# Kernel optimization log

Measured on AMD Instinct MI355X. Metric: run time of the kernel, lower is better.

The kernel has to match this reference:

```python
import jax, jax.numpy as jnp
import numpy as np

T, N, G2, R, E, I, O = 20, 512, 16, 128, 64, 2, 5


def setup_inputs() -> dict:
    key = jax.random.key(0)
    ks = jax.random.split(key, 12)
    s = 0.02
    return {
        "nodes": jax.random.normal(ks[0], (T, N, I), jnp.float32),
        "grids": jax.random.uniform(ks[1], (T, N, N, G2), jnp.float32),
        "hidden_states": jnp.zeros((N, R), jnp.float32),
        "cell_states": jnp.zeros((N, R), jnp.float32),
        "W_in": jax.random.normal(ks[2], (E, I), jnp.float32) * s,
        "b_in": jnp.zeros((E,), jnp.float32),
        "W_tensor": jax.random.normal(ks[3], (E, G2 * R), jnp.float32) * s,
        "b_tensor": jnp.zeros((E,), jnp.float32),
        "W_ih": jax.random.normal(ks[4], (4 * R, 2 * E), jnp.float32) * s,
        "b_ih": jnp.zeros((4 * R,), jnp.float32),
        "W_hh": jax.random.normal(ks[5], (4 * R, R), jnp.float32) * s,
        "b_hh": jnp.zeros((4 * R,), jnp.float32),
        "W_out": jax.random.normal(ks[6], (O, R), jnp.float32) * s,
        "b_out": jnp.zeros((O,), jnp.float32),
    }


def reference(nodes, grids, hidden_states, cell_states,
              W_in, b_in, W_tensor, b_tensor,
              W_ih, b_ih, W_hh, b_hh, W_out, b_out):
    def step(carry, xs):
        h, c = carry
        nodes_t, grid_t = xs  # [N,I], [N,N,G2]
        # social tensor: for each node, grid[node].T @ hidden -> [N, G2, R]
        social = jnp.einsum('nmg,mr->ngr', grid_t, h).reshape(N, G2 * R)
        ie = jax.nn.relu(nodes_t @ W_in.T + b_in)          # [N,E]
        te = jax.nn.relu(social @ W_tensor.T + b_tensor)   # [N,E]
        x = jnp.concatenate([ie, te], axis=1)              # [N,2E]
        gates = x @ W_ih.T + b_ih + h @ W_hh.T + b_hh      # [N,4R]
        i_g, f_g, g_g, o_g = jnp.split(gates, 4, axis=1)   # torch LSTMCell order
        c2 = jax.nn.sigmoid(f_g) * c + jax.nn.sigmoid(i_g) * jnp.tanh(g_g)
        h2 = jax.nn.sigmoid(o_g) * jnp.tanh(c2)
        out = h2 @ W_out.T + b_out                         # [N,O]
        return (h2, c2), out

    (h_f, c_f), outputs = jax.lax.scan(step, (hidden_states, cell_states), (nodes, grids))
    return outputs, h_f, c_f
```

## Files before the change

kernel.cpp:

```cpp
#include <hip/hip_runtime.h>

#define TT 20
#define NNODE 512
#define G2C 16
#define RCH 128
#define ECH 64
#define ICH 2
#define OCH 5
#define KSOC 8192
#define KSPLIT 16
#define KCH 512
#define SGS 516

#define OFF_H    0u
#define OFF_C    65536u
#define OFF_HT   131072u
#define OFF_PART 655360u
#define OFF_WCAT 1179648u
#define OFF_WTT  1310720u
#define OFF_BS   1441792u

__device__ __forceinline__ double sigd(double x){ return 1.0/(1.0+exp(-x)); }

__global__ void k_init(const float* __restrict__ h0, const float* __restrict__ c0,
                       const float* __restrict__ W_ih, const float* __restrict__ b_ih,
                       const float* __restrict__ W_hh, const float* __restrict__ b_hh,
                       const float* __restrict__ W_tensor, double* __restrict__ ws) {
  int tid = blockIdx.x*blockDim.x + threadIdx.x;
  int nthr = gridDim.x*blockDim.x;
  double* h = ws + OFF_H; double* c = ws + OFF_C;
  double* Wcat = ws + OFF_WCAT; double* WtT = ws + OFF_WTT;
  double* bs = ws + OFF_BS;
  for (int i = tid; i < NNODE*RCH; i += nthr) { h[i] = (double)h0[i]; c[i] = (double)c0[i]; }
  for (int i = tid; i < 512*256; i += nthr) {
    int kk = i & 255; int gc = i >> 8;
    Wcat[i] = (kk < 128) ? (double)W_ih[gc*128 + kk] : (double)W_hh[gc*128 + (kk-128)];
  }
  for (int i = tid; i < 2048*64; i += nthr) {
    int e = i & 63; int q2 = i >> 6;
    WtT[i] = (double)W_tensor[e*2048 + q2];
  }
  for (int i = tid; i < 512; i += nthr) bs[i] = (double)b_ih[i] + (double)b_hh[i];
}

__global__ __launch_bounds__(256) void k_social(const float* __restrict__ grids,
                                                double* __restrict__ ws, int t) {
  __shared__ __align__(16) double sgd[4160];
  float* sgf = (float*)sgd;
  const double* __restrict__ Ht = ws + OFF_HT;
  double* __restrict__ part = ws + OFF_PART;
  const int kc = blockIdx.x & (KSPLIT-1);
  const int n0 = (blockIdx.x >> 4) << 4;
  const int kb = kc * KCH;
  const int tid = threadIdx.x;
  const float* gbase = grids + (size_t)t*NNODE*KSOC;
  for (int i = tid; i < 16*128; i += 256) {
    int row = i >> 7; int c4 = i & 127;
    float4 v = *(const float4*)(gbase + (size_t)(n0+row)*KSOC + kb + (c4<<2));
    *(float4*)(&sgf[row*SGS + (c4<<2)]) = v;
  }
  __syncthreads();
  const int lane = tid & 63;
  const int wv = tid >> 6;
  const int e0 = (lane & 15) << 2;
  const int nq = lane >> 4;
  double acc[4][4] = {};
  const int kl0 = wv << 7;
  const double* htp = Ht + (size_t)(kb + kl0)*ECH + e0;
  #pragma unroll 2
  for (int kk = 0; kk < 128; kk += 2) {
    double2 b0a = *(const double2*)(htp + (size_t)kk*ECH);
    double2 b0b = *(const double2*)(htp + (size_t)kk*ECH + 2);
    double2 b1a = *(const double2*)(htp + (size_t)(kk+1)*ECH);
    double2 b1b = *(const double2*)(htp + (size_t)(kk+1)*ECH + 2);
    const int kl = kl0 + kk;
    #pragma unroll
    for (int jn = 0; jn < 4; ++jn) {
      float2 av2 = *(const float2*)(&sgf[((jn<<2)+nq)*SGS + kl]);
      double a0 = (double)av2.x, a1 = (double)av2.y;
      acc[jn][0] += a0*b0a.x + a1*b1a.x;
      acc[jn][1] += a0*b0a.y + a1*b1a.y;
      acc[jn][2] += a0*b0b.x + a1*b1b.x;
      acc[jn][3] += a0*b0b.y + a1*b1b.y;
    }
  }
  __syncthreads();
  if (wv > 0) {
    double* rp = sgd + ((size_t)(wv-1)*64 + lane)*16;
    #pragma unroll
    for (int jn = 0; jn < 4; ++jn)
      #pragma unroll
      for (int je = 0; je < 4; ++je) rp[(jn<<2)+je] = acc[jn][je];
  }
  __syncthreads();
  if (wv == 0) {
    #pragma unroll
    for (int w = 0; w < 3; ++w) {
      const double* rp = sgd + ((size_t)w*64 + lane)*16;
      #pragma unroll
      for (int jn = 0; jn < 4; ++jn)
        #pragma unroll
        for (int je = 0; je < 4; ++je) acc[jn][je] += rp[(jn<<2)+je];
    }
    #pragma unroll
    for (int jn = 0; jn < 4; ++jn) {
      double* pp = part + ((size_t)kc*NNODE + n0 + (jn<<2) + nq)*ECH + e0;
      pp[0]=acc[jn][0]; pp[1]=acc[jn][1]; pp[2]=acc[jn][2]; pp[3]=acc[jn][3];
    }
  }
}

__global__ __launch_bounds__(256) void k_cell(const float* __restrict__ nodes,
    const float* __restrict__ W_in, const float* __restrict__ b_in,
    const float* __restrict__ b_tensor,
    double* __restrict__ ws, float* __restrict__ hf, float* __restrict__ cf, int t) {
  __shared__ double xh[16][258];
  __shared__ double gbuf[32][17];
  double* __restrict__ h = ws + OFF_H;
  double* __restrict__ c = ws + OFF_C;
  const double* __restrict__ part = ws + OFF_PART;
  const double* __restrict__ Wcat = ws + OFF_WCAT;
  const double* __restrict__ bs = ws + OFF_BS;
  const int tid = threadIdx.x;
  const int nc = blockIdx.x >> 4;
  const int rc = blockIdx.x & 15;
  const int m0 = nc << 4;
  {
    const int e = tid & 63;
    #pragma unroll
    for (int pass = 0; pass < 4; ++pass) {
      const int n = (tid >> 6) + (pass << 2);
      const int m = m0 + n;
      double te = (double)b_tensor[e];
      for (int kc = 0; kc < KSPLIT; ++kc)
        te += part[((size_t)kc*NNODE + m)*ECH + e];
      double n0v = (double)nodes[((size_t)t*NNODE + m)*ICH + 0];
      double n1v = (double)nodes[((size_t)t*NNODE + m)*ICH + 1];
      double ie = n0v*(double)W_in[e*2] + n1v*(double)W_in[e*2+1] + (double)b_in[e];
      xh[n][e] = fmax(ie, 0.0);
      xh[n][64+e] = fmax(te, 0.0);
    }
    const int r = tid & 127;
    #pragma unroll
    for (int pass = 0; pass < 8; ++pass) {
      const int n = (tid >> 7) + (pass << 1);
      xh[n][128+r] = h[(size_t)(m0+n)*RCH + r];
    }
  }
  __syncthreads();
  {
    const int n = tid & 15, tg = tid >> 4;
    const int q0 = tg >> 3, jr = tg & 7;
    const int gc0 = q0*128 + rc*8 + jr;
    const int gc1 = (q0+2)*128 + rc*8 + jr;
    const double* w0 = Wcat + (size_t)gc0*256;
    const double* w1 = Wcat + (size_t)gc1*256;
    double a0 = 0.0, a1 = 0.0;
    #pragma unroll 8
    for (int kk = 0; kk < 256; kk += 2) {
      double2 xv = *(const double2*)(&xh[n][kk]);
      double2 wa = *(const double2*)(w0 + kk);
      double2 wb = *(const double2*)(w1 + kk);
      a0 += xv.x*wa.x + xv.y*wa.y;
      a1 += xv.x*wb.x + xv.y*wb.y;
    }
    gbuf[tg][n]    = a0 + bs[gc0];
    gbuf[tg+16][n] = a1 + bs[gc1];
  }
  __syncthreads();
  if (tid < 128) {
    const int n = tid >> 3, jr = tid & 7;
    const int m = m0 + n, r = rc*8 + jr;
    double ig = sigd(gbuf[jr][n]);
    double fg = sigd(gbuf[8+jr][n]);
    double gg = tanh(gbuf[16+jr][n]);
    double og = sigd(gbuf[24+jr][n]);
    double cold = c[(size_t)m*RCH + r];
    double c2 = fg*cold + ig*gg;
    double h2v = og*tanh(c2);
    c[(size_t)m*RCH + r] = c2;
    h[(size_t)m*RCH + r] = h2v;
    if (t == TT-1) {
      hf[(size_t)m*RCH + r] = (float)h2v;
      cf[(size_t)m*RCH + r] = (float)c2;
    }
  }
}

__global__ __launch_bounds__(256) void k_ht_out(const float* __restrict__ W_out,
    const float* __restrict__ b_out, double* __restrict__ ws,
    float* __restrict__ outp, int t, int wout) {
  __shared__ double h2b[16][130];
  const double* __restrict__ h = ws + OFF_H;
  const double* __restrict__ WtT = ws + OFF_WTT;
  double* __restrict__ Ht = ws + OFF_HT;
  const int tid = threadIdx.x;
  const int mc = blockIdx.x >> 3;
  const int gc2 = blockIdx.x & 7;
  const int m0 = mc << 4, g0 = gc2 << 1;
  {
    const int r = tid & 127;
    #pragma unroll
    for (int pass = 0; pass < 8; ++pass) {
      const int n = (tid >> 7) + (pass << 1);
      h2b[n][r] = h[(size_t)(m0+n)*RCH + r];
    }
  }
  __syncthreads();
  {
    const int e = tid & 63, mh = tid >> 6;
    const double* wt0 = WtT + (size_t)(g0*128)*ECH + e;
    const double* wt1 = WtT + (size_t)((g0+1)*128)*ECH + e;
    double acc[4][2] = {};
    #pragma unroll 4
    for (int rr = 0; rr < 128; ++rr) {
      double w0 = wt0[(size_t)rr*ECH];
      double w1 = wt1[(size_t)rr*ECH];
      #pragma unroll
      for (int mi = 0; mi < 4; ++mi) {
        double hv = h2b[(mh<<2)+mi][rr];
        acc[mi][0] += hv*w0;
        acc[mi][1] += hv*w1;
      }
    }
    #pragma unroll
    for (int mi = 0; mi < 4; ++mi) {
      const int m = m0 + (mh<<2) + mi;
      Ht[((size_t)m*G2C + g0    )*ECH + e] = acc[mi][0];
      Ht[((size_t)m*G2C + g0 + 1)*ECH + e] = acc[mi][1];
    }
  }
  if (gc2 == 0 && wout && tid < 80) {
    const int mi = tid / OCH, oo = tid % OCH;
    double v = (double)b_out[oo];
    for (int r = 0; r < 128; ++r)
      v += h2b[mi][r]*(double)W_out[oo*RCH + r];
    outp[((size_t)t*NNODE + m0 + mi)*OCH + oo] = (float)v;
  }
}

extern "C" void kernel_launch(void* const* d_in, const int* in_sizes, int n_in,
                              void* d_out, int out_size, void* d_ws, size_t ws_size,
                              hipStream_t stream) {
  const float* nodes    = (const float*)d_in[0];
  const float* grids    = (const float*)d_in[1];
  const float* h0       = (const float*)d_in[2];
  const float* c0       = (const float*)d_in[3];
  const float* W_in     = (const float*)d_in[4];
  const float* b_in     = (const float*)d_in[5];
  const float* W_tensor = (const float*)d_in[6];
  const float* b_tensor = (const float*)d_in[7];
  const float* W_ih     = (const float*)d_in[8];
  const float* b_ih     = (const float*)d_in[9];
  const float* W_hh     = (const float*)d_in[10];
  const float* b_hh     = (const float*)d_in[11];
  const float* W_out    = (const float*)d_in[12];
  const float* b_out    = (const float*)d_in[13];
  double* ws = (double*)d_ws;
  float* outp = (float*)d_out;
  float* hf = outp + (size_t)TT*NNODE*OCH;
  float* cf = hf + (size_t)NNODE*RCH;

  k_init<<<256, 256, 0, stream>>>(h0, c0, W_ih, b_ih, W_hh, b_hh, W_tensor, ws);
  k_ht_out<<<256, 256, 0, stream>>>(W_out, b_out, ws, outp, 0, 0);
  for (int t = 0; t < TT; ++t) {
    k_social<<<512, 256, 0, stream>>>(grids, ws, t);
    k_cell<<<512, 256, 0, stream>>>(nodes, W_in, b_in, b_tensor, ws, hf, cf, t);
    k_ht_out<<<256, 256, 0, stream>>>(W_out, b_out, ws, outp, t, 1);
  }
}
```

Baseline: 1.397 ms.

## Fuse per-step kernels into one persistent kernel with atomic grid barriers

Replaces the 61 per-timestep kernel launches (social, cell, ht_out) with one persistent 512-block kernel that loops over timesteps and separates phases with a global atomic-counter barrier. The Ht projection is also remapped to one g-slice per block across 512 blocks, and it is skipped on the last step. This removes launch overhead and inter-kernel gaps. In exchange, all 512 blocks must be co-resident, since otherwise the spin barrier deadlocks, and the barriers add spin and fence costs.

```diff
diff --git a/kernel.cpp b/kernel.cpp
--- a/kernel.cpp
+++ b/kernel.cpp
@@ -11,6 +11,7 @@
 #define KSPLIT 16
 #define KCH 512
 #define SGS 516
+#define NBLK 512
 
 #define OFF_H    0u
 #define OFF_C    65536u
@@ -19,6 +20,7 @@
 #define OFF_WCAT 1179648u
 #define OFF_WTT  1310720u
 #define OFF_BS   1441792u
+#define OFF_BAR  1442304u
 
 __device__ __forceinline__ double sigd(double x){ return 1.0/(1.0+exp(-x)); }
 
@@ -31,6 +33,7 @@
   double* h = ws + OFF_H; double* c = ws + OFF_C;
   double* Wcat = ws + OFF_WCAT; double* WtT = ws + OFF_WTT;
   double* bs = ws + OFF_BS;
+  if (tid == 0) { unsigned* bar = (unsigned*)(ws + OFF_BAR); bar[0] = 0u; bar[1] = 0u; }
   for (int i = tid; i < NNODE*RCH; i += nthr) { h[i] = (double)h0[i]; c[i] = (double)c0[i]; }
   for (int i = tid; i < 512*256; i += nthr) {
     int kk = i & 255; int gc = i >> 8;
@@ -43,199 +46,237 @@
   for (int i = tid; i < 512; i += nthr) bs[i] = (double)b_ih[i] + (double)b_hh[i];
 }
 
-__global__ __launch_bounds__(256) void k_social(const float* __restrict__ grids,
-                                                double* __restrict__ ws, int t) {
-  __shared__ __align__(16) double sgd[4160];
-  float* sgf = (float*)sgd;
-  const double* __restrict__ Ht = ws + OFF_HT;
-  double* __restrict__ part = ws + OFF_PART;
-  const int kc = blockIdx.x & (KSPLIT-1);
-  const int n0 = (blockIdx.x >> 4) << 4;
-  const int kb = kc * KCH;
-  const int tid = threadIdx.x;
-  const float* gbase = grids + (size_t)t*NNODE*KSOC;
-  for (int i = tid; i < 16*128; i += 256) {
-    int row = i >> 7; int c4 = i & 127;
-    float4 v = *(const float4*)(gbase + (size_t)(n0+row)*KSOC + kb + (c4<<2));
-    *(float4*)(&sgf[row*SGS + (c4<<2)]) = v;
-  }
+__device__ __forceinline__ void grid_sync(unsigned* bar, unsigned gen) {
   __syncthreads();
-  const int lane = tid & 63;
-  const int wv = tid >> 6;
-  const int e0 = (lane & 15) << 2;
-  const int nq = lane >> 4;
-  double acc[4][4] = {};
-  const int kl0 = wv << 7;
-  const double* htp = Ht + (size_t)(kb + kl0)*ECH + e0;
-  #pragma unroll 2
-  for (int kk = 0; kk < 128; kk += 2) {
-    double2 b0a = *(const double2*)(htp + (size_t)kk*ECH);
-    double2 b0b = *(const double2*)(htp + (size_t)kk*ECH + 2);
-    double2 b1a = *(const double2*)(htp + (size_t)(kk+1)*ECH);
-    double2 b1b = *(const double2*)(htp + (size_t)(kk+1)*ECH + 2);
-    const int kl = kl0 + kk;
-    #pragma unroll
-    for (int jn = 0; jn < 4; ++jn) {
-      float2 av2 = *(const float2*)(&sgf[((jn<<2)+nq)*SGS + kl]);
-      double a0 = (double)av2.x, a1 = (double)av2.y;
-      acc[jn][0] += a0*b0a.x + a1*b1a.x;
-      acc[jn][1] += a0*b0a.y + a1*b1a.y;
-      acc[jn][2] += a0*b0b.x + a1*b1b.x;
-      acc[jn][3] += a0*b0b.y + a1*b1b.y;
+  if (threadIdx.x == 0) {
+    unsigned prev = __hip_atomic_fetch_add(&bar[0], 1u, __ATOMIC_ACQ_REL,
+                                           __HIP_MEMORY_SCOPE_AGENT);
+    if (prev == NBLK-1u) {
+      __hip_atomic_store(&bar[0], 0u, __ATOMIC_RELAXED, __HIP_MEMORY_SCOPE_AGENT);
+      __hip_atomic_store(&bar[1], gen+1u, __ATOMIC_RELEASE, __HIP_MEMORY_SCOPE_AGENT);
+    } else {
+      while (__hip_atomic_load(&bar[1], __ATOMIC_ACQUIRE,
+                               __HIP_MEMORY_SCOPE_AGENT) != gen+1u)
+        __builtin_amdgcn_s_sleep(2);
     }
   }
   __syncthreads();
-  if (wv > 0) {
-    double* rp = sgd + ((size_t)(wv-1)*64 + lane)*16;
-    #pragma unroll
-    for (int jn = 0; jn < 4; ++jn)
-      #pragma unroll
-      for (int je = 0; je < 4; ++je) rp[(jn<<2)+je] = acc[jn][je];
-  }
-  __syncthreads();
-  if (wv == 0) {
-    #pragma unroll
-    for (int w = 0; w < 3; ++w) {
-      const double* rp = sgd + ((size_t)w*64 + lane)*16;
-      #pragma unroll
-      for (int jn = 0; jn < 4; ++jn)
-        #pragma unroll
-        for (int je = 0; je < 4; ++je) acc[jn][je] += rp[(jn<<2)+je];
-    }
-    #pragma unroll
-    for (int jn = 0; jn < 4; ++jn) {
-      double* pp = part + ((size_t)kc*NNODE + n0 + (jn<<2) + nq)*ECH + e0;
-      pp[0]=acc[jn][0]; pp[1]=acc[jn][1]; pp[2]=acc[jn][2]; pp[3]=acc[jn][3];
-    }
-  }
 }
 
-__global__ __launch_bounds__(256) void k_cell(const float* __restrict__ nodes,
+__global__ __launch_bounds__(256, 2) void k_steps(
+    const float* __restrict__ nodes, const float* __restrict__ grids,
     const float* __restrict__ W_in, const float* __restrict__ b_in,
     const float* __restrict__ b_tensor,
-    double* __restrict__ ws, float* __restrict__ hf, float* __restrict__ cf, int t) {
-  __shared__ double xh[16][258];
-  __shared__ double gbuf[32][17];
+    const float* __restrict__ W_out, const float* __restrict__ b_out,
+    double* __restrict__ ws, float* __restrict__ outp,
+    float* __restrict__ hf, float* __restrict__ cf) {
+  __shared__ __align__(16) double smem[4672];
   double* __restrict__ h = ws + OFF_H;
   double* __restrict__ c = ws + OFF_C;
-  const double* __restrict__ part = ws + OFF_PART;
+  double* __restrict__ Ht = ws + OFF_HT;
+  double* __restrict__ part = ws + OFF_PART;
   const double* __restrict__ Wcat = ws + OFF_WCAT;
+  const double* __restrict__ WtT = ws + OFF_WTT;
   const double* __restrict__ bs = ws + OFF_BS;
+  unsigned* bar = (unsigned*)(ws + OFF_BAR);
   const int tid = threadIdx.x;
-  const int nc = blockIdx.x >> 4;
-  const int rc = blockIdx.x & 15;
-  const int m0 = nc << 4;
+  const int bid = blockIdx.x;
+  unsigned gen = 0;
+
   {
-    const int e = tid & 63;
-    #pragma unroll
-    for (int pass = 0; pass < 4; ++pass) {
-      const int n = (tid >> 6) + (pass << 2);
-      const int m = m0 + n;
-      double te = (double)b_tensor[e];
-      for (int kc = 0; kc < KSPLIT; ++kc)
-        te += part[((size_t)kc*NNODE + m)*ECH + e];
-      double n0v = (double)nodes[((size_t)t*NNODE + m)*ICH + 0];
-      double n1v = (double)nodes[((size_t)t*NNODE + m)*ICH + 1];
-      double ie = n0v*(double)W_in[e*2] + n1v*(double)W_in[e*2+1] + (double)b_in[e];
-      xh[n][e] = fmax(ie, 0.0);
-      xh[n][64+e] = fmax(te, 0.0);
-    }
-    const int r = tid & 127;
-    #pragma unroll
-    for (int pass = 0; pass < 8; ++pass) {
-      const int n = (tid >> 7) + (pass << 1);
-      xh[n][128+r] = h[(size_t)(m0+n)*RCH + r];
-    }
-  }
-  __syncthreads();
-  {
-    const int n = tid & 15, tg = tid >> 4;
-    const int q0 = tg >> 3, jr = tg & 7;
-    const int gc0 = q0*128 + rc*8 + jr;
-    const int gc1 = (q0+2)*128 + rc*8 + jr;
-    const double* w0 = Wcat + (size_t)gc0*256;
-    const double* w1 = Wcat + (size_t)gc1*256;
-    double a0 = 0.0, a1 = 0.0;
-    #pragma unroll 8
-    for (int kk = 0; kk < 256; kk += 2) {
-      double2 xv = *(const double2*)(&xh[n][kk]);
-      double2 wa = *(const double2*)(w0 + kk);
-      double2 wb = *(const double2*)(w1 + kk);
-      a0 += xv.x*wa.x + xv.y*wa.y;
-      a1 += xv.x*wb.x + xv.y*wb.y;
-    }
-    gbuf[tg][n]    = a0 + bs[gc0];
-    gbuf[tg+16][n] = a1 + bs[gc1];
-  }
-  __syncthreads();
-  if (tid < 128) {
-    const int n = tid >> 3, jr = tid & 7;
-    const int m = m0 + n, r = rc*8 + jr;
-    double ig = sigd(gbuf[jr][n]);
-    double fg = sigd(gbuf[8+jr][n]);
-    double gg = tanh(gbuf[16+jr][n]);
-    double og = sigd(gbuf[24+jr][n]);
-    double cold = c[(size_t)m*RCH + r];
-    double c2 = fg*cold + ig*gg;
-    double h2v = og*tanh(c2);
-    c[(size_t)m*RCH + r] = c2;
-    h[(size_t)m*RCH + r] = h2v;
-    if (t == TT-1) {
-      hf[(size_t)m*RCH + r] = (float)h2v;
-      cf[(size_t)m*RCH + r] = (float)c2;
-    }
-  }
-}
-
-__global__ __launch_bounds__(256) void k_ht_out(const float* __restrict__ W_out,
-    const float* __restrict__ b_out, double* __restrict__ ws,
-    float* __restrict__ outp, int t, int wout) {
-  __shared__ double h2b[16][130];
-  const double* __restrict__ h = ws + OFF_H;
-  const double* __restrict__ WtT = ws + OFF_WTT;
-  double* __restrict__ Ht = ws + OFF_HT;
-  const int tid = threadIdx.x;
-  const int mc = blockIdx.x >> 3;
-  const int gc2 = blockIdx.x & 7;
-  const int m0 = mc << 4, g0 = gc2 << 1;
-  {
+    double (*h2b)[130] = (double(*)[130])smem;
+    const int mc = bid >> 4, g = bid & 15;
+    const int m0 = mc << 4;
     const int r = tid & 127;
     #pragma unroll
     for (int pass = 0; pass < 8; ++pass) {
       const int n = (tid >> 7) + (pass << 1);
       h2b[n][r] = h[(size_t)(m0+n)*RCH + r];
     }
-  }
-  __syncthreads();
-  {
+    __syncthreads();
     const int e = tid & 63, mh = tid >> 6;
-    const double* wt0 = WtT + (size_t)(g0*128)*ECH + e;
-    const double* wt1 = WtT + (size_t)((g0+1)*128)*ECH + e;
-    double acc[4][2] = {};
+    const double* wt = WtT + (size_t)(g*128)*ECH + e;
+    double acc[4] = {};
     #pragma unroll 4
     for (int rr = 0; rr < 128; ++rr) {
-      double w0 = wt0[(size_t)rr*ECH];
-      double w1 = wt1[(size_t)rr*ECH];
+      double w0 = wt[(size_t)rr*ECH];
       #pragma unroll
-      for (int mi = 0; mi < 4; ++mi) {
-        double hv = h2b[(mh<<2)+mi][rr];
-        acc[mi][0] += hv*w0;
-        acc[mi][1] += hv*w1;
-      }
+      for (int mi = 0; mi < 4; ++mi) acc[mi] += h2b[(mh<<2)+mi][rr]*w0;
     }
     #pragma unroll
-    for (int mi = 0; mi < 4; ++mi) {
-      const int m = m0 + (mh<<2) + mi;
-      Ht[((size_t)m*G2C + g0    )*ECH + e] = acc[mi][0];
-      Ht[((size_t)m*G2C + g0 + 1)*ECH + e] = acc[mi][1];
-    }
-  }
-  if (gc2 == 0 && wout && tid < 80) {
-    const int mi = tid / OCH, oo = tid % OCH;
-    double v = (double)b_out[oo];
-    for (int r = 0; r < 128; ++r)
-      v += h2b[mi][r]*(double)W_out[oo*RCH + r];
-    outp[((size_t)t*NNODE + m0 + mi)*OCH + oo] = (float)v;
+    for (int mi = 0; mi < 4; ++mi)
+      Ht[((size_t)(m0+(mh<<2)+mi)*G2C + g)*ECH + e] = acc[mi];
+  }
+  grid_sync(bar, gen); ++gen;
+
+  for (int t = 0; t < TT; ++t) {
+    {
+      float* sgf = (float*)smem;
+      const int kc = bid & (KSPLIT-1);
+      const int n0 = (bid >> 4) << 4;
+      const int kb = kc * KCH;
+      const float* gbase = grids + (size_t)t*NNODE*KSOC;
+      for (int i = tid; i < 16*128; i += 256) {
+        int row = i >> 7; int c4 = i & 127;
+        float4 v = *(const float4*)(gbase + (size_t)(n0+row)*KSOC + kb + (c4<<2));
+        *(float4*)(&sgf[row*SGS + (c4<<2)]) = v;
+      }
+      __syncthreads();
+      const int lane = tid & 63;
+      const int wv = tid >> 6;
+      const int e0 = (lane & 15) << 2;
+      const int nq = lane >> 4;
+      double acc[4][4] = {};
+      const int kl0 = wv << 7;
+      const double* htp = Ht + (size_t)(kb + kl0)*ECH + e0;
+      #pragma unroll 2
+      for (int kk = 0; kk < 128; kk += 2) {
+        double2 b0a = *(const double2*)(htp + (size_t)kk*ECH);
+        double2 b0b = *(const double2*)(htp + (size_t)kk*ECH + 2);
+        double2 b1a = *(const double2*)(htp + (size_t)(kk+1)*ECH);
+        double2 b1b = *(const double2*)(htp + (size_t)(kk+1)*ECH + 2);
+        const int kl = kl0 + kk;
+        #pragma unroll
+        for (int jn = 0; jn < 4; ++jn) {
+          float2 av2 = *(const float2*)(&sgf[((jn<<2)+nq)*SGS + kl]);
+          double a0 = (double)av2.x, a1 = (double)av2.y;
+          acc[jn][0] += a0*b0a.x + a1*b1a.x;
+          acc[jn][1] += a0*b0a.y + a1*b1a.y;
+          acc[jn][2] += a0*b0b.x + a1*b1b.x;
+          acc[jn][3] += a0*b0b.y + a1*b1b.y;
+        }
+      }
+      __syncthreads();
+      if (wv > 0) {
+        double* rp = smem + ((size_t)(wv-1)*64 + lane)*16;
+        #pragma unroll
+        for (int jn = 0; jn < 4; ++jn)
+          #pragma unroll
+          for (int je = 0; je < 4; ++je) rp[(jn<<2)+je] = acc[jn][je];
+      }
+      __syncthreads();
+      if (wv == 0) {
+        #pragma unroll
+        for (int w = 0; w < 3; ++w) {
+          const double* rp = smem + ((size_t)w*64 + lane)*16;
+          #pragma unroll
+          for (int jn = 0; jn < 4; ++jn)
+            #pragma unroll
+            for (int je = 0; je < 4; ++je) acc[jn][je] += rp[(jn<<2)+je];
+        }
+        #pragma unroll
+        for (int jn = 0; jn < 4; ++jn) {
+          double* pp = part + ((size_t)kc*NNODE + n0 + (jn<<2) + nq)*ECH + e0;
+          pp[0]=acc[jn][0]; pp[1]=acc[jn][1]; pp[2]=acc[jn][2]; pp[3]=acc[jn][3];
+        }
+      }
+    }
+    grid_sync(bar, gen); ++gen;
+
+    {
+      double (*xh)[258] = (double(*)[258])smem;
+      double (*gbuf)[17] = (double(*)[17])(smem + 4128);
+      const int nc = bid >> 4;
+      const int rc = bid & 15;
+      const int m0 = nc << 4;
+      {
+        const int e = tid & 63;
+        #pragma unroll
+        for (int pass = 0; pass < 4; ++pass) {
+          const int n = (tid >> 6) + (pass << 2);
+          const int m = m0 + n;
+          double te = (double)b_tensor[e];
+          for (int kc = 0; kc < KSPLIT; ++kc)
+            te += part[((size_t)kc*NNODE + m)*ECH + e];
+          double n0v = (double)nodes[((size_t)t*NNODE + m)*ICH + 0];
+          double n1v = (double)nodes[((size_t)t*NNODE + m)*ICH + 1];
+          double ie = n0v*(double)W_in[e*2] + n1v*(double)W_in[e*2+1] + (double)b_in[e];
+          xh[n][e] = fmax(ie, 0.0);
+          xh[n][64+e] = fmax(te, 0.0);
+        }
+        const int r = tid & 127;
+        #pragma unroll
+        for (int pass = 0; pass < 8; ++pass) {
+          const int n = (tid >> 7) + (pass << 1);
+          xh[n][128+r] = h[(size_t)(m0+n)*RCH + r];
+        }
+      }
+      __syncthreads();
+      {
+        const int n = tid & 15, tg = tid >> 4;
+        const int q0 = tg >> 3, jr = tg & 7;
+        const int gc0 = q0*128 + rc*8 + jr;
+        const int gc1 = (q0+2)*128 + rc*8 + jr;
+        const double* w0 = Wcat + (size_t)gc0*256;
+        const double* w1 = Wcat + (size_t)gc1*256;
+        double a0 = 0.0, a1 = 0.0;
+        #pragma unroll 8
+        for (int kk = 0; kk < 256; kk += 2) {
+          double2 xv = *(const double2*)(&xh[n][kk]);
+          double2 wa = *(const double2*)(w0 + kk);
+          double2 wb = *(const double2*)(w1 + kk);
+          a0 += xv.x*wa.x + xv.y*wa.y;
+          a1 += xv.x*wb.x + xv.y*wb.y;
+        }
+        gbuf[tg][n]    = a0 + bs[gc0];
+        gbuf[tg+16][n] = a1 + bs[gc1];
+      }
+      __syncthreads();
+      if (tid < 128) {
+        const int n = tid >> 3, jr = tid & 7;
+        const int m = m0 + n, r = rc*8 + jr;
+        double ig = sigd(gbuf[jr][n]);
+        double fg = sigd(gbuf[8+jr][n]);
+        double gg = tanh(gbuf[16+jr][n]);
+        double og = sigd(gbuf[24+jr][n]);
+        double cold = c[(size_t)m*RCH + r];
+        double c2 = fg*cold + ig*gg;
+        double h2v = og*tanh(c2);
+        c[(size_t)m*RCH + r] = c2;
+        h[(size_t)m*RCH + r] = h2v;
+        if (t == TT-1) {
+          hf[(size_t)m*RCH + r] = (float)h2v;
+          cf[(size_t)m*RCH + r] = (float)c2;
+        }
+      }
+    }
+    grid_sync(bar, gen); ++gen;
+
+    {
+      double (*h2b)[130] = (double(*)[130])smem;
+      const int mc = bid >> 4, g = bid & 15;
+      const int m0 = mc << 4;
+      const int r = tid & 127;
+      #pragma unroll
+      for (int pass = 0; pass < 8; ++pass) {
+        const int n = (tid >> 7) + (pass << 1);
+        h2b[n][r] = h[(size_t)(m0+n)*RCH + r];
+      }
+      __syncthreads();
+      if (t < TT-1) {
+        const int e = tid & 63, mh = tid >> 6;
+        const double* wt = WtT + (size_t)(g*128)*ECH + e;
+        double acc[4] = {};
+        #pragma unroll 4
+        for (int rr = 0; rr < 128; ++rr) {
+          double w0 = wt[(size_t)rr*ECH];
+          #pragma unroll
+          for (int mi = 0; mi < 4; ++mi) acc[mi] += h2b[(mh<<2)+mi][rr]*w0;
+        }
+        #pragma unroll
+        for (int mi = 0; mi < 4; ++mi)
+          Ht[((size_t)(m0+(mh<<2)+mi)*G2C + g)*ECH + e] = acc[mi];
+      }
+      if (g == 0 && tid < 80) {
+        const int mi = tid / OCH, oo = tid % OCH;
+        double v = (double)b_out[oo];
+        #pragma unroll 8
+        for (int r2 = 0; r2 < 128; ++r2)
+          v += h2b[mi][r2]*(double)W_out[oo*RCH + r2];
+        outp[((size_t)t*NNODE + m0 + mi)*OCH + oo] = (float)v;
+      }
+    }
+    if (t < TT-1) { grid_sync(bar, gen); ++gen; }
   }
 }
 
@@ -262,10 +303,6 @@
   float* cf = hf + (size_t)NNODE*RCH;
 
   k_init<<<256, 256, 0, stream>>>(h0, c0, W_ih, b_ih, W_hh, b_hh, W_tensor, ws);
-  k_ht_out<<<256, 256, 0, stream>>>(W_out, b_out, ws, outp, 0, 0);
-  for (int t = 0; t < TT; ++t) {
-    k_social<<<512, 256, 0, stream>>>(grids, ws, t);
-    k_cell<<<512, 256, 0, stream>>>(nodes, W_in, b_in, b_tensor, ws, hf, cf, t);
-    k_ht_out<<<256, 256, 0, stream>>>(W_out, b_out, ws, outp, t, 1);
-  }
+  k_steps<<<NBLK, 256, 0, stream>>>(nodes, grids, W_in, b_in, b_tensor,
+                                    W_out, b_out, ws, outp, hf, cf);
 }
```

After: 5.463 ms. +291.1%, slower.

## Fuse LSTM cell update with Ht projection and output into one kernel

Applied to the files above, without the earlier changes.

Merges the per-step cell kernel and the Ht/output projection kernel into one kernel where each block handles two nodes fully: all four gates per thread, the cell update, then the projection of the new hidden state through W_tensor and W_out. This drops one launch per timestep and avoids writing h to global memory only to read it back. The Ht projection for the last step is skipped because nothing uses it, and a separate initial Ht kernel is added. In exchange, each block now reads the full Wcat and WtT weight matrices for only two nodes, which sharply lowers weight reuse and raises global and L2 traffic. Grid size also falls from 512 to 256 blocks.

```diff
diff --git a/kernel.cpp b/kernel.cpp
--- a/kernel.cpp
+++ b/kernel.cpp
@@ -41,6 +41,47 @@
     WtT[i] = (double)W_tensor[e*2048 + q2];
   }
   for (int i = tid; i < 512; i += nthr) bs[i] = (double)b_ih[i] + (double)b_hh[i];
+}
+
+__global__ __launch_bounds__(256) void k_ht0(double* __restrict__ ws) {
+  __shared__ double h2b[16][130];
+  const double* __restrict__ h = ws + OFF_H;
+  const double* __restrict__ WtT = ws + OFF_WTT;
+  double* __restrict__ Ht = ws + OFF_HT;
+  const int tid = threadIdx.x;
+  const int mc = blockIdx.x >> 3;
+  const int gc2 = blockIdx.x & 7;
+  const int m0 = mc << 4, g0 = gc2 << 1;
+  {
+    const int r = tid & 127;
+    #pragma unroll
+    for (int pass = 0; pass < 8; ++pass) {
+      const int n = (tid >> 7) + (pass << 1);
+      h2b[n][r] = h[(size_t)(m0+n)*RCH + r];
+    }
+  }
+  __syncthreads();
+  const int e = tid & 63, mh = tid >> 6;
+  const double* wt0 = WtT + (size_t)(g0*128)*ECH + e;
+  const double* wt1 = WtT + (size_t)((g0+1)*128)*ECH + e;
+  double acc[4][2] = {};
+  #pragma unroll 4
+  for (int rr = 0; rr < 128; ++rr) {
+    double w0 = wt0[(size_t)rr*ECH];
+    double w1 = wt1[(size_t)rr*ECH];
+    #pragma unroll
+    for (int mi = 0; mi < 4; ++mi) {
+      double hv = h2b[(mh<<2)+mi][rr];
+      acc[mi][0] += hv*w0;
+      acc[mi][1] += hv*w1;
+    }
+  }
+  #pragma unroll
+  for (int mi = 0; mi < 4; ++mi) {
+    const int m = m0 + (mh<<2) + mi;
+    Ht[((size_t)m*G2C + g0    )*ECH + e] = acc[mi][0];
+    Ht[((size_t)m*G2C + g0 + 1)*ECH + e] = acc[mi][1];
+  }
 }
 
 __global__ __launch_bounds__(256) void k_social(const float* __restrict__ grids,
@@ -110,131 +151,98 @@
   }
 }
 
-__global__ __launch_bounds__(256) void k_cell(const float* __restrict__ nodes,
+__global__ __launch_bounds__(256) void k_cellht(const float* __restrict__ nodes,
     const float* __restrict__ W_in, const float* __restrict__ b_in,
     const float* __restrict__ b_tensor,
-    double* __restrict__ ws, float* __restrict__ hf, float* __restrict__ cf, int t) {
-  __shared__ double xh[16][258];
-  __shared__ double gbuf[32][17];
+    const float* __restrict__ W_out, const float* __restrict__ b_out,
+    double* __restrict__ ws, float* __restrict__ outp,
+    float* __restrict__ hf, float* __restrict__ cf, int t) {
+  __shared__ double xh[2][258];
+  __shared__ double h2b[2][130];
   double* __restrict__ h = ws + OFF_H;
   double* __restrict__ c = ws + OFF_C;
+  double* __restrict__ Ht = ws + OFF_HT;
   const double* __restrict__ part = ws + OFF_PART;
   const double* __restrict__ Wcat = ws + OFF_WCAT;
+  const double* __restrict__ WtT = ws + OFF_WTT;
   const double* __restrict__ bs = ws + OFF_BS;
   const int tid = threadIdx.x;
-  const int nc = blockIdx.x >> 4;
-  const int rc = blockIdx.x & 15;
-  const int m0 = nc << 4;
+  const int m0 = blockIdx.x << 1;
+  if (tid < 128) {
+    const int n = tid >> 6, e = tid & 63;
+    const int m = m0 + n;
+    double te = (double)b_tensor[e];
+    for (int kc = 0; kc < KSPLIT; ++kc)
+      te += part[((size_t)kc*NNODE + m)*ECH + e];
+    double n0v = (double)nodes[((size_t)t*NNODE + m)*ICH + 0];
+    double n1v = (double)nodes[((size_t)t*NNODE + m)*ICH + 1];
+    double ie = n0v*(double)W_in[e*2] + n1v*(double)W_in[e*2+1] + (double)b_in[e];
+    xh[n][e] = fmax(ie, 0.0);
+    xh[n][64+e] = fmax(te, 0.0);
+  }
   {
-    const int e = tid & 63;
-    #pragma unroll
-    for (int pass = 0; pass < 4; ++pass) {
-      const int n = (tid >> 6) + (pass << 2);
-      const int m = m0 + n;
-      double te = (double)b_tensor[e];
-      for (int kc = 0; kc < KSPLIT; ++kc)
-        te += part[((size_t)kc*NNODE + m)*ECH + e];
-      double n0v = (double)nodes[((size_t)t*NNODE + m)*ICH + 0];
-      double n1v = (double)nodes[((size_t)t*NNODE + m)*ICH + 1];
-      double ie = n0v*(double)W_in[e*2] + n1v*(double)W_in[e*2+1] + (double)b_in[e];
-      xh[n][e] = fmax(ie, 0.0);
-      xh[n][64+e] = fmax(te, 0.0);
-    }
-    const int r = tid & 127;
-    #pragma unroll
-    for (int pass = 0; pass < 8; ++pass) {
-      const int n = (tid >> 7) + (pass << 1);
-      xh[n][128+r] = h[(size_t)(m0+n)*RCH + r];
-    }
+    const int n = tid >> 7, r = tid & 127;
+    xh[n][128+r] = h[(size_t)(m0+n)*RCH + r];
   }
   __syncthreads();
   {
-    const int n = tid & 15, tg = tid >> 4;
-    const int q0 = tg >> 3, jr = tg & 7;
-    const int gc0 = q0*128 + rc*8 + jr;
-    const int gc1 = (q0+2)*128 + rc*8 + jr;
-    const double* w0 = Wcat + (size_t)gc0*256;
-    const double* w1 = Wcat + (size_t)gc1*256;
-    double a0 = 0.0, a1 = 0.0;
+    const int n = tid >> 7, r = tid & 127;
+    const int m = m0 + n;
+    const double* wA = Wcat + ((size_t)(      r) << 8);
+    const double* wB = Wcat + ((size_t)(128 + r) << 8);
+    const double* wC = Wcat + ((size_t)(256 + r) << 8);
+    const double* wD = Wcat + ((size_t)(384 + r) << 8);
+    double a0 = 0.0, a1 = 0.0, a2 = 0.0, a3 = 0.0;
     #pragma unroll 8
     for (int kk = 0; kk < 256; kk += 2) {
       double2 xv = *(const double2*)(&xh[n][kk]);
-      double2 wa = *(const double2*)(w0 + kk);
-      double2 wb = *(const double2*)(w1 + kk);
+      double2 wa = *(const double2*)(wA + kk);
+      double2 wb = *(const double2*)(wB + kk);
+      double2 wc = *(const double2*)(wC + kk);
+      double2 wd = *(const double2*)(wD + kk);
       a0 += xv.x*wa.x + xv.y*wa.y;
       a1 += xv.x*wb.x + xv.y*wb.y;
-    }
-    gbuf[tg][n]    = a0 + bs[gc0];
-    gbuf[tg+16][n] = a1 + bs[gc1];
-  }
-  __syncthreads();
-  if (tid < 128) {
-    const int n = tid >> 3, jr = tid & 7;
-    const int m = m0 + n, r = rc*8 + jr;
-    double ig = sigd(gbuf[jr][n]);
-    double fg = sigd(gbuf[8+jr][n]);
-    double gg = tanh(gbuf[16+jr][n]);
-    double og = sigd(gbuf[24+jr][n]);
+      a2 += xv.x*wc.x + xv.y*wc.y;
+      a3 += xv.x*wd.x + xv.y*wd.y;
+    }
+    double ig = sigd(a0 + bs[r]);
+    double fg = sigd(a1 + bs[128+r]);
+    double gg = tanh(a2 + bs[256+r]);
+    double og = sigd(a3 + bs[384+r]);
     double cold = c[(size_t)m*RCH + r];
     double c2 = fg*cold + ig*gg;
     double h2v = og*tanh(c2);
     c[(size_t)m*RCH + r] = c2;
     h[(size_t)m*RCH + r] = h2v;
+    h2b[n][r] = h2v;
     if (t == TT-1) {
       hf[(size_t)m*RCH + r] = (float)h2v;
       cf[(size_t)m*RCH + r] = (float)c2;
     }
   }
-}
-
-__global__ __launch_bounds__(256) void k_ht_out(const float* __restrict__ W_out,
-    const float* __restrict__ b_out, double* __restrict__ ws,
-    float* __restrict__ outp, int t, int wout) {
-  __shared__ double h2b[16][130];
-  const double* __restrict__ h = ws + OFF_H;
-  const double* __restrict__ WtT = ws + OFF_WTT;
-  double* __restrict__ Ht = ws + OFF_HT;
-  const int tid = threadIdx.x;
-  const int mc = blockIdx.x >> 3;
-  const int gc2 = blockIdx.x & 7;
-  const int m0 = mc << 4, g0 = gc2 << 1;
-  {
-    const int r = tid & 127;
-    #pragma unroll
-    for (int pass = 0; pass < 8; ++pass) {
-      const int n = (tid >> 7) + (pass << 1);
-      h2b[n][r] = h[(size_t)(m0+n)*RCH + r];
-    }
-  }
-  __syncthreads();
-  {
-    const int e = tid & 63, mh = tid >> 6;
-    const double* wt0 = WtT + (size_t)(g0*128)*ECH + e;
-    const double* wt1 = WtT + (size_t)((g0+1)*128)*ECH + e;
-    double acc[4][2] = {};
-    #pragma unroll 4
-    for (int rr = 0; rr < 128; ++rr) {
-      double w0 = wt0[(size_t)rr*ECH];
-      double w1 = wt1[(size_t)rr*ECH];
-      #pragma unroll
-      for (int mi = 0; mi < 4; ++mi) {
-        double hv = h2b[(mh<<2)+mi][rr];
-        acc[mi][0] += hv*w0;
-        acc[mi][1] += hv*w1;
-      }
-    }
-    #pragma unroll
-    for (int mi = 0; mi < 4; ++mi) {
-      const int m = m0 + (mh<<2) + mi;
-      Ht[((size_t)m*G2C + g0    )*ECH + e] = acc[mi][0];
-      Ht[((size_t)m*G2C + g0 + 1)*ECH + e] = acc[mi][1];
-    }
-  }
-  if (gc2 == 0 && wout && tid < 80) {
+  __syncthreads();
+  if (t < TT-1) {
+    const int e = tid & 63;
+    const int slot = tid >> 6;
+    const int mi = slot >> 1;
+    const int g8 = (slot & 1) << 3;
+    #pragma unroll
+    for (int j = 0; j < 8; ++j) {
+      const int g = g8 + j;
+      const double* wt = WtT + (size_t)(g*128)*ECH + e;
+      double acc = 0.0;
+      #pragma unroll 4
+      for (int rr = 0; rr < 128; ++rr)
+        acc += h2b[mi][rr] * wt[(size_t)rr*ECH];
+      Ht[((size_t)(m0+mi)*G2C + g)*ECH + e] = acc;
+    }
+  }
+  if (tid < 2*OCH) {
     const int mi = tid / OCH, oo = tid % OCH;
     double v = (double)b_out[oo];
-    for (int r = 0; r < 128; ++r)
-      v += h2b[mi][r]*(double)W_out[oo*RCH + r];
+    #pragma unroll 8
+    for (int r2 = 0; r2 < 128; ++r2)
+      v += h2b[mi][r2]*(double)W_out[oo*RCH + r2];
     outp[((size_t)t*NNODE + m0 + mi)*OCH + oo] = (float)v;
   }
 }
@@ -262,10 +270,10 @@
   float* cf = hf + (size_t)NNODE*RCH;
 
   k_init<<<256, 256, 0, stream>>>(h0, c0, W_ih, b_ih, W_hh, b_hh, W_tensor, ws);
-  k_ht_out<<<256, 256, 0, stream>>>(W_out, b_out, ws, outp, 0, 0);
+  k_ht0<<<256, 256, 0, stream>>>(ws);
   for (int t = 0; t < TT; ++t) {
     k_social<<<512, 256, 0, stream>>>(grids, ws, t);
-    k_cell<<<512, 256, 0, stream>>>(nodes, W_in, b_in, b_tensor, ws, hf, cf, t);
-    k_ht_out<<<256, 256, 0, stream>>>(W_out, b_out, ws, outp, t, 1);
-  }
-}
+    k_cellht<<<256, 256, 0, stream>>>(nodes, W_in, b_in, b_tensor, W_out, b_out,
+                                      ws, outp, hf, cf, t);
+  }
+}
```

After: 3.384 ms. +142.2%, slower.
